# Optimization experiments

Measured on AMD Instinct MI355X. Metric: run time of the kernel, lower is better.

Reference implementation:

```python
import jax, jax.numpy as jnp
import numpy as np

# Dimensions (see shape_source)
B, D, Q, M = 2, 1024, 1024, 1024
K = Q + M                      # klen = mlen + qlen
N_HEAD, D_HEAD = 16, 64        # n_head * d_head == d_model
D_INNER = 4096
LOCAL_SIZE = 1000              # Attention: self.local_size or 1000
EPS = 1e-5                     # F.layer_norm default eps


def setup_inputs() -> dict:
    key = jax.random.key(0)
    ks = jax.random.split(key, 12)
    z = jax.random.normal(ks[0], (B, D, Q), jnp.float32)
    z_hist = jax.random.normal(ks[1], (B, D, M), jnp.float32)
    u = jax.random.normal(ks[2], (B, 3 * N_HEAD * D_HEAD, K), jnp.float32) * 0.1
    # sinusoidal relative position embedding (PositionalEmbedding), positions K-1..0
    inv_freq = 1.0 / (10000.0 ** (jnp.arange(0, D, 2, dtype=jnp.float32) / D))
    pos_seq = jnp.arange(K - 1, -1, -1, dtype=jnp.float32)
    sinusoid = inv_freq[:, None] * pos_seq[None, :]  # (D/2, K)
    pos_emb = jnp.concatenate([jnp.sin(sinusoid), jnp.cos(sinusoid)], axis=0)[None]  # (1, D, K)
    s = 0.02
    W_qkv = jax.random.normal(ks[3], (3 * N_HEAD * D_HEAD, D), jnp.float32) * s
    W_r = jax.random.normal(ks[4], (N_HEAD * D_HEAD, D), jnp.float32) * s
    r_w_bias = jax.random.uniform(ks[5], (N_HEAD, D_HEAD), jnp.float32, -0.05, 0.05)
    r_r_bias = jax.random.uniform(ks[6], (N_HEAD, D_HEAD), jnp.float32, -0.05, 0.05)
    W_o = jax.random.normal(ks[7], (D, N_HEAD * D_HEAD), jnp.float32) * s
    b_o = jnp.zeros((D,), jnp.float32)
    W_ff1 = jax.random.normal(ks[8], (D_INNER, D), jnp.float32) * s
    b_ff1 = jnp.zeros((D_INNER,), jnp.float32)
    W_ff2 = jax.random.normal(ks[9], (D, D_INNER), jnp.float32) * s
    b_ff2 = jnp.zeros((D,), jnp.float32)
    return dict(z=z, z_hist=z_hist, u=u, pos_emb=pos_emb, W_qkv=W_qkv, W_r=W_r,
                r_w_bias=r_w_bias, r_r_bias=r_r_bias, W_o=W_o, b_o=b_o,
                W_ff1=W_ff1, b_ff1=b_ff1, W_ff2=W_ff2, b_ff2=b_ff2)


def _ln(x, axis):
    # F.layer_norm without affine params
    mu = jnp.mean(x, axis=axis, keepdims=True)
    var = jnp.var(x, axis=axis, keepdims=True)
    return (x - mu) / jnp.sqrt(var + EPS)


def _rel_shift(x):
    # Transformer-XL relative shift: pad left on key dim, reinterpret, drop row.
    b, n, q, k = x.shape
    x = jnp.pad(x, ((0, 0), (0, 0), (0, 0), (1, 0)))
    x = x.reshape(b, n, k + 1, q)
    return x[:, :, 1:, :].reshape(b, n, q, k)


def reference(z, z_hist, u, pos_emb, W_qkv, W_r, r_w_bias, r_r_bias, W_o, b_o,
              W_ff1, b_ff1, W_ff2, b_ff2):
    scale = 1.0 / (D_HEAD ** 0.5)
    # ---- Attention (post-LN, Conv1d kernel=1 == pointwise matmul) ----
    cat = jnp.concatenate([z_hist, z], axis=2)                 # (B, D, K)
    w_heads = jnp.einsum('od,bdk->bok', W_qkv, cat) + u        # (B, 3*n*dh, K)
    q_h, k_h, v_h = jnp.split(w_heads, 3, axis=1)
    q_h = q_h[:, :, -Q:].reshape(B, N_HEAD, D_HEAD, Q)
    k_h = k_h.reshape(B, N_HEAD, D_HEAD, K)
    v_h = v_h.reshape(B, N_HEAD, D_HEAD, K)
    r_k = jnp.einsum('od,dk->ok', W_r, pos_emb[0]).reshape(N_HEAD, D_HEAD, K)
    AC = jnp.einsum('bndi,bndj->bnij', q_h + r_w_bias[:, :, None], k_h)
    BD = _rel_shift(jnp.einsum('bndi,ndj->bnij', q_h + r_r_bias[:, :, None], r_k))
    score = (AC + BD) * scale                                  # (B, n, Q, K)
    causal = jnp.triu(jnp.ones((Q, K), bool), k=1 + M)         # future tokens
    local = jnp.tril(jnp.ones((Q, K), bool), k=M - LOCAL_SIZE)  # beyond local window
    mask = causal | local
    score = jnp.where(mask[None, None], -jnp.inf, score)
    prob = jax.nn.softmax(score, axis=-1)
    attn_vec = jnp.einsum('bnij,bndj->bndi', prob, v_h).reshape(B, N_HEAD * D_HEAD, Q)
    attn_out = jnp.einsum('od,bdq->boq', W_o, attn_vec) + b_o[None, :, None]
    out = _ln(attn_out + z, axis=1)                            # LN over d_model (dim=1)
    # ---- FFN (operates token-major) ----
    h = out.transpose(0, 2, 1)                                 # (B, Q, D)
    ff = jnp.maximum(h @ W_ff1.T + b_ff1, 0.0) @ W_ff2.T + b_ff2
    y = _ln(ff + h, axis=-1)
    return y.transpose(0, 2, 1)                                # (B, D, Q)
```

## Files before the change

kernel.cpp:

```cpp
#include <hip/hip_runtime.h>

#define D_MODEL 1024
#define QLEN 1024

typedef __bf16 bf16x8 __attribute__((ext_vector_type(8)));
typedef __bf16 bf16x4 __attribute__((ext_vector_type(4)));
typedef float f32x4 __attribute__((ext_vector_type(4)));

__device__ __forceinline__ void gload16(const void* g, void* l) {
    __builtin_amdgcn_global_load_lds(
        (const __attribute__((address_space(1))) void*)g,
        (__attribute__((address_space(3))) void*)l, 16, 0, 0);
}

__device__ __forceinline__ void gemm_core8(
    __bf16* __restrict__ smA, __bf16* __restrict__ smB,
    const __bf16* __restrict__ A, const __bf16* __restrict__ Bt,
    float* __restrict__ C, __bf16* __restrict__ Cb,
    const float* __restrict__ U, const float* __restrict__ Ut,
    const float* __restrict__ bias,
    int K, int lda, int ldb, int ldC, int ldU, int relu, int m0, int n0)
{
    const int t = threadIdx.x;
    const int lane = t & 63, w = t >> 6;
    const int l15 = lane & 15, lg = lane >> 4;
    const int wm = w >> 2, wn = w & 3;
    const int srow = lane >> 3, cpr = lane & 7;
    const int NK = K >> 6;
    const int SZ = 128 * 64;

    #define STAGE(buf, kt)                                                                   \
    {                                                                                        \
        int k0s = (kt) * 64;                                                                 \
        _Pragma("unroll")                                                                    \
        for (int i = 0; i < 2; ++i) {                                                        \
            int r = w * 16 + i * 8 + srow;                                                   \
            int c = cpr ^ (r & 7);                                                           \
            gload16(&A[(long long)(m0 + r) * lda + k0s + c * 8],                             \
                    &smA[(buf) * SZ + (w * 16 + i * 8) * 64]);                               \
            gload16(&Bt[(long long)(n0 + r) * ldb + k0s + c * 8],                            \
                    &smB[(buf) * SZ + (w * 16 + i * 8) * 64]);                               \
        }                                                                                    \
    }

    f32x4 acc[4][2] = {};
    STAGE(0, 0);

    for (int kt = 0; kt < NK; ++kt) {
        const int cb = kt & 1;
        if (kt + 1 < NK) {
            STAGE(cb ^ 1, kt + 1);
            asm volatile("s_waitcnt vmcnt(4)" ::: "memory");
        } else {
            asm volatile("s_waitcnt vmcnt(0)" ::: "memory");
        }
        __builtin_amdgcn_sched_barrier(0);
        __builtin_amdgcn_s_barrier();

        #pragma unroll
        for (int kk = 0; kk < 2; ++kk) {
            bf16x8 bfr[2];
            #pragma unroll
            for (int nt = 0; nt < 2; ++nt) {
                int nr = wn * 32 + nt * 16 + l15;
                bfr[nt] = *(const bf16x8*)&smB[cb * SZ + nr * 64 + (((kk * 4 + lg) ^ (nr & 7)) * 8)];
            }
            #pragma unroll
            for (int mt = 0; mt < 4; ++mt) {
                int mr = wm * 64 + mt * 16 + l15;
                bf16x8 afr = *(const bf16x8*)&smA[cb * SZ + mr * 64 + (((kk * 4 + lg) ^ (mr & 7)) * 8)];
                #pragma unroll
                for (int nt = 0; nt < 2; ++nt)
                    acc[mt][nt] = __builtin_amdgcn_mfma_f32_16x16x32_bf16(afr, bfr[nt], acc[mt][nt], 0, 0, 0);
            }
        }
        asm volatile("s_waitcnt lgkmcnt(0)" ::: "memory");
        __builtin_amdgcn_sched_barrier(0);
        __builtin_amdgcn_s_barrier();
    }
    #undef STAGE

    if (Ut) {
        float* uf = (float*)smA;
        #pragma unroll
        for (int hh = 0; hh < 2; ++hh) {
            __syncthreads();
            int r = t >> 3, c0 = (t & 7) * 16;
            const float* src = &Ut[(long long)(n0 + hh * 64 + r) * ldU + m0 + c0];
            #pragma unroll
            for (int k = 0; k < 4; ++k)
                *(float4*)&uf[r * 132 + c0 + k * 4] = *(const float4*)&src[k * 4];
            __syncthreads();
            if ((wn >> 1) == hh) {
                #pragma unroll
                for (int nt = 0; nt < 2; ++nt) {
                    int rr = wn * 32 + nt * 16 + l15 - hh * 64;
                    #pragma unroll
                    for (int mt = 0; mt < 4; ++mt) {
                        #pragma unroll
                        for (int rg = 0; rg < 4; ++rg) {
                            int m = wm * 64 + mt * 16 + lg * 4 + rg;
                            acc[mt][nt][rg] += uf[rr * 132 + m];
                        }
                    }
                }
            }
        }
    }

    #pragma unroll
    for (int mt = 0; mt < 4; ++mt) {
        #pragma unroll
        for (int nt = 0; nt < 2; ++nt) {
            #pragma unroll
            for (int rg = 0; rg < 4; ++rg) {
                int m = m0 + wm * 64 + mt * 16 + lg * 4 + rg;
                int n = n0 + wn * 32 + nt * 16 + l15;
                float v = acc[mt][nt][rg];
                if (U)    v += U[(long long)m * ldU + n];
                if (bias) v += bias[n];
                if (relu) v = fmaxf(v, 0.0f);
                if (Cb) Cb[(long long)m * ldC + n] = (__bf16)v;
                else    C [(long long)m * ldC + n] = v;
            }
        }
    }
}

template<int KSPLIT>
__global__ __launch_bounds__(512) void gemm_bf16_k(
    const __bf16* __restrict__ A, const __bf16* __restrict__ Bt,
    float* __restrict__ C0, float* __restrict__ C1,
    __bf16* __restrict__ Cb,
    const float* __restrict__ U, const float* __restrict__ bias,
    int K, int lda, int ldb, int ldC, int ldU, int relu)
{
    __shared__ __bf16 SM[32768];
    int yb = blockIdx.y;
    int half = 0;
    if (KSPLIT > 1) { half = yb & (KSPLIT - 1); yb /= KSPLIT; }
    const int Keff = K / KSPLIT;
    A  += (long long)half * Keff;
    Bt += (long long)half * Keff;
    float* C = half ? C1 : C0;
    if (half) { bias = nullptr; U = nullptr; }
    gemm_core8(SM, SM + 16384, A, Bt, C, Cb, U, nullptr, bias,
               Keff, lda, ldb, ldC, ldU, relu, yb * 128, blockIdx.x * 128);
}

__global__ __launch_bounds__(512) void gemm_fused3(
    const __bf16* __restrict__ cat_t, const __bf16* __restrict__ Wqkvb,
    __bf16* __restrict__ qkT, const float* __restrict__ u,
    __bf16* __restrict__ wh_v,
    const __bf16* __restrict__ pos_t, const __bf16* __restrict__ Wrb,
    __bf16* __restrict__ rkT)
{
    __shared__ __bf16 SM[32768];
    int bid = blockIdx.x;
    if (bid < 512) {
        int zz = bid >> 8, rem = bid & 255, y = rem >> 4, x = rem & 15;
        gemm_core8(SM, SM + 16384,
                   cat_t + (long long)zz * 2097152, Wqkvb,
                   nullptr, qkT + (long long)zz * 4194304,
                   nullptr, u + (long long)zz * 6291456, nullptr,
                   1024, 1024, 1024, 2048, 2048, 0, y * 128, x * 128);
    } else if (bid < 768) {
        int l = bid - 512, zz = l >> 7, rem = l & 127, y = rem >> 4, x = rem & 15;
        gemm_core8(SM, SM + 16384,
                   Wqkvb + 2048 * 1024, cat_t + (long long)zz * 2097152,
                   nullptr, wh_v + (long long)zz * 2097152,
                   u + 4194304 + (long long)zz * 6291456, nullptr, nullptr,
                   1024, 1024, 1024, 2048, 2048, 0, y * 128, x * 128);
    } else {
        int l = bid - 768, y = l >> 3, x = l & 7;
        gemm_core8(SM, SM + 16384,
                   pos_t + 960 * 1024, Wrb,
                   nullptr, rkT, nullptr, nullptr, nullptr,
                   1024, 1024, 1024, 1024, 0, 0, y * 128, x * 128);
    }
}

__global__ __launch_bounds__(256) void prep_all(
    const float* __restrict__ Wqkv, __bf16* __restrict__ Wqkvb,
    const float* __restrict__ Wr,   __bf16* __restrict__ Wrb,
    const float* __restrict__ Wo,   __bf16* __restrict__ Wob,
    const float* __restrict__ Wff1, __bf16* __restrict__ Wff1b,
    const float* __restrict__ Wff2, __bf16* __restrict__ Wff2b,
    const float* __restrict__ zh, const float* __restrict__ z, __bf16* __restrict__ cat_t,
    const float* __restrict__ pos, __bf16* __restrict__ pos_t)
{
    __shared__ float ts[32][33];
    int bid = blockIdx.x;
    const int t = threadIdx.x;
    if (bid < 13312) {
        long long i = ((long long)bid * 256 + t) * 4;
        const float* s; __bf16* dd;
        if (i < 3145728)                    { s = Wqkv + i; dd = Wqkvb + i; }
        else if ((i -= 3145728) < 1048576)  { s = Wr + i;   dd = Wrb + i; }
        else if ((i -= 1048576) < 1048576)  { s = Wo + i;   dd = Wob + i; }
        else if ((i -= 1048576) < 4194304)  { s = Wff1 + i; dd = Wff1b + i; }
        else { i -= 4194304;                  s = Wff2 + i; dd = Wff2b + i; }
        float4 v = *(const float4*)s;
        bf16x4 o = { (__bf16)v.x, (__bf16)v.y, (__bf16)v.z, (__bf16)v.w };
        *(bf16x4*)dd = o;
        return;
    }
    bid -= 13312;
    const float* S; __bf16* D; int R, Cc, bx, by;
    if (bid < 2048) {
        int zz = bid >> 10, r2 = bid & 1023;
        S = zh + (long long)zz * 1048576; D = cat_t + (long long)zz * 2097152;
        R = 1024; Cc = 1024; bx = r2 & 31; by = r2 >> 5;
    } else if (bid < 4096) {
        int l = bid - 2048; int zz = l >> 10, r2 = l & 1023;
        S = z + (long long)zz * 1048576; D = cat_t + 1048576 + (long long)zz * 2097152;
        R = 1024; Cc = 1024; bx = r2 & 31; by = r2 >> 5;
    } else if (bid < 6144) {
        int l = bid - 4096;
        S = pos; D = pos_t; R = 1024; Cc = 2048; bx = l & 63; by = l >> 6;
    } else {
        int l = bid - 6144;
        int i = (l * 256 + t) * 4;
        bf16x4 zv = { (__bf16)0.f, (__bf16)0.f, (__bf16)0.f, (__bf16)0.f };
        *(bf16x4*)&pos_t[2048 * 1024 + i] = zv;
        return;
    }
    int r0 = by * 32, c0 = bx * 32;
    int tr = t >> 5, tc = t & 31;
    #pragma unroll
    for (int p = 0; p < 4; ++p)
        ts[tr + p * 8][tc] = S[(long long)(r0 + tr + p * 8) * Cc + c0 + tc];
    __syncthreads();
    #pragma unroll
    for (int p = 0; p < 4; ++p)
        D[(long long)(c0 + tr + p * 8) * R + r0 + tc] = (__bf16)ts[tc][tr + p * 8];
}

__global__ __launch_bounds__(512) void attn_mfma(
    const __bf16* __restrict__ QKT, const __bf16* __restrict__ WHV,
    const __bf16* __restrict__ RKT,
    const float* __restrict__ rwb, const float* __restrict__ rrb,
    __bf16* __restrict__ AVt)
{
    __shared__ __bf16 SM[51712];
    __bf16* KT0 = SM;
    __bf16* KT1 = SM + 4096;
    __bf16* VS0 = SM + 8192;
    __bf16* VS1 = SM + 12288;
    __bf16* RT  = SM + 16384;
    __bf16* PS  = SM + 32768;
    __bf16* BT  = SM + 40960;

    const int d = blockIdx.x;
    const int xcd = d & 7, idx = d >> 3;
    const int qt = idx & 7;
    const int gq = xcd + 8 * (idx >> 3);
    const int b = gq >> 4, n = gq & 15;
    const int i0 = qt * 128;

    const int t = threadIdx.x;
    const int lane = t & 63, w = t >> 6;
    const int l15 = lane & 15, lg = lane >> 4;
    const int g = w >> 2, wg = w & 3;
    const int fco = n * 64;

    const __bf16* qkb = QKT + (long long)b * (2048 * 2048);
    const __bf16* vb  = WHV + (long long)b * (1024 * 2048) + (long long)fco * 2048;
    __bf16* BTw = BT + w * 1344;

    #pragma unroll
    for (int pp = 0; pp < 2; ++pp) {
        int cid = pp * 512 + t;
        int q = cid >> 3, s = cid & 7, c = s ^ (q & 7);
        bf16x8 qv = *(const bf16x8*)&qkb[(long long)(1024 + i0 + q) * 2048 + fco + c * 8];
        bf16x8 ow, orr;
        #pragma unroll
        for (int e = 0; e < 8; ++e) {
            float qf = (float)qv[e];
            ow[e]  = (__bf16)(qf + rwb[fco + c * 8 + e]);
            orr[e] = (__bf16)(qf + rrb[fco + c * 8 + e]);
        }
        *(bf16x8*)&PS[q * 64 + s * 8] = ow;
        *(bf16x8*)&RT[q * 64 + s * 8] = orr;
    }
    __syncthreads();

    #define LDF(buf, row, ch) (*(const bf16x8*)&(buf)[(row) * 64 + ((((ch) ^ ((row) & 7))) * 8)])

    const int mrow = w * 16 + l15;
    bf16x8 qw0 = LDF(PS, mrow, lg), qw1 = LDF(PS, mrow, lg + 4);
    bf16x8 qr0 = LDF(RT, mrow, lg), qr1 = LDF(RT, mrow, lg + 4);
    asm volatile("s_waitcnt lgkmcnt(0)" ::: "memory");
    __builtin_amdgcn_sched_barrier(0);
    __builtin_amdgcn_s_barrier();

    {
        int r = t >> 3, s = t & 7, c = s ^ (r & 7);
        gload16(&qkb[(long long)(i0 + r) * 2048 + 1024 + fco + c * 8], &KT0[(w * 8) * 64]);
        gload16(&vb[(long long)r * 2048 + i0 + c * 8], &VS0[(w * 8) * 64]);
        #pragma unroll
        for (int pp = 0; pp < 3; ++pp) {
            int cid = pp * 512 + t;
            int rr = cid >> 3, ss = cid & 7, cc = ss ^ (rr & 7);
            gload16(&RKT[(long long)rr * 1024 + fco + cc * 8], &RT[(pp * 64 + w * 8) * 64]);
        }
    }
    asm volatile("s_waitcnt vmcnt(0)" ::: "memory");
    __builtin_amdgcn_sched_barrier(0);
    __builtin_amdgcn_s_barrier();

    const bf16x8 ones = { (__bf16)1.f, (__bf16)1.f, (__bf16)1.f, (__bf16)1.f,
                          (__bf16)1.f, (__bf16)1.f, (__bf16)1.f, (__bf16)1.f };

    f32x4 O0 = {}, O1 = {}, O2 = {}, O3 = {};
    float rm[4] = {-1e30f, -1e30f, -1e30f, -1e30f};
    float rl[4] = {0.f, 0.f, 0.f, 0.f};
    int cur = 0;

    for (int kt = 0; kt <= 17; ++kt) {
        __bf16* KTc = cur ? KT1 : KT0;
        __bf16* VSc = cur ? VS1 : VS0;
        __bf16* KTn = cur ? KT0 : KT1;
        __bf16* VSn = cur ? VS0 : VS1;
        const int ktr = kt - g;

        if (kt < 17) {
            int j0n = i0 + (kt + 1) * 64;
            int r = t >> 3, s = t & 7, c = s ^ (r & 7);
            gload16(&qkb[(long long)(j0n + r) * 2048 + 1024 + fco + c * 8], &KTn[(w * 8) * 64]);
            gload16(&vb[(long long)r * 2048 + j0n + c * 8], &VSn[(w * 8) * 64]);
        }
        if (kt < 16) {
            int rb = kt * 64 + 128;
            int lb = ((kt + 2) & 3) * 64;
            int r = t >> 3, s = t & 7, c = s ^ (r & 7);
            gload16(&RKT[(long long)(rb + r) * 1024 + fco + c * 8], &RT[(lb + w * 8) * 64]);
        }
        __builtin_amdgcn_sched_barrier(0);

        __builtin_amdgcn_s_setprio(1);
        #pragma unroll
        for (int k5 = 0; k5 < 5; ++k5) {
            int pr = (3 - wg + k5) * 16 + l15;
            int lr = ((ktr * 64) + pr) & 255;
            const __bf16* rrow = &RT[lr * 64];
            f32x4 cc = {};
            cc = __builtin_amdgcn_mfma_f32_16x16x32_bf16(qr0, *(const bf16x8*)&rrow[((lg ^ (pr & 7)) * 8)], cc, 0, 0, 0);
            cc = __builtin_amdgcn_mfma_f32_16x16x32_bf16(qr1, *(const bf16x8*)&rrow[(((lg + 4) ^ (pr & 7)) * 8)], cc, 0, 0, 0);
            #pragma unroll
            for (int rg = 0; rg < 4; ++rg)
                BTw[(lg * 4 + rg) * 84 + k5 * 16 + l15] = (__bf16)cc[rg];
        }
        __builtin_amdgcn_s_setprio(0);

        f32x4 cc4[4];
        __builtin_amdgcn_s_setprio(1);
        #pragma unroll
        for (int nt = 0; nt < 4; ++nt) {
            int jr = nt * 16 + l15;
            f32x4 cc = {};
            cc = __builtin_amdgcn_mfma_f32_16x16x32_bf16(qw0, LDF(KTc, jr, lg), cc, 0, 0, 0);
            cc = __builtin_amdgcn_mfma_f32_16x16x32_bf16(qw1, LDF(KTc, jr, lg + 4), cc, 0, 0, 0);
            cc4[nt] = cc;
        }
        __builtin_amdgcn_s_setprio(0);

        const bool bnd = (ktr <= 1) | (ktr >= 16);
        float sv[4][4];
        if (!bnd) {
            #pragma unroll
            for (int nt = 0; nt < 4; ++nt) {
                int jr = nt * 16 + l15;
                #pragma unroll
                for (int rg = 0; rg < 4; ++rg) {
                    int r4 = lg * 4 + rg;
                    sv[nt][rg] = (cc4[nt][rg] + (float)BTw[r4 * 84 + jr - r4 + 15]) * 0.125f;
                }
            }
        } else {
            #pragma unroll
            for (int nt = 0; nt < 4; ++nt) {
                int jr = nt * 16 + l15;
                #pragma unroll
                for (int rg = 0; rg < 4; ++rg) {
                    int r4 = lg * 4 + rg;
                    int dji = jr - (wg * 16 + r4);
                    float s = (cc4[nt][rg] + (float)BTw[r4 * 84 + jr - r4 + 15]) * 0.125f;
                    bool valid = (ktr == 0) ? (dji >= 25)
                               : (ktr == 1) ? (dji >= -39)
                               : (ktr == 16) ? (dji <= 0) : false;
                    sv[nt][rg] = valid ? s : -1e30f;
                }
            }
        }

        float lmax[4];
        bool need = false;
        #pragma unroll
        for (int rg = 0; rg < 4; ++rg) {
            lmax[rg] = fmaxf(fmaxf(sv[0][rg], sv[1][rg]), fmaxf(sv[2][rg], sv[3][rg]));
            need = need || (lmax[rg] > rm[rg] + 8.0f);
        }
        if (__any(need)) {
            #pragma unroll
            for (int rg = 0; rg < 4; ++rg) {
                float m = lmax[rg];
                m = fmaxf(m, __shfl_xor(m, 1, 16));
                m = fmaxf(m, __shfl_xor(m, 2, 16));
                m = fmaxf(m, __shfl_xor(m, 4, 16));
                m = fmaxf(m, __shfl_xor(m, 8, 16));
                float nm = fmaxf(rm[rg], m);
                float fac = __expf(rm[rg] - nm);
                rm[rg] = nm;
                rl[rg] *= fac;
                O0[rg] *= fac; O1[rg] *= fac; O2[rg] *= fac; O3[rg] *= fac;
            }
        }

        if (!bnd) {
            #pragma unroll
            for (int nt = 0; nt < 4; ++nt) {
                int jc = nt * 16 + l15;
                #pragma unroll
                for (int rg = 0; rg < 4; ++rg) {
                    float p = __expf(sv[nt][rg] - rm[rg]);
                    int row = w * 16 + lg * 4 + rg;
                    PS[row * 64 + (((jc >> 3) ^ (row & 7)) * 8) + (jc & 7)] = (__bf16)p;
                }
            }
        } else {
            #pragma unroll
            for (int nt = 0; nt < 4; ++nt) {
                int jc = nt * 16 + l15;
                #pragma unroll
                for (int rg = 0; rg < 4; ++rg) {
                    float p = (sv[nt][rg] > -1e29f) ? __expf(sv[nt][rg] - rm[rg]) : 0.0f;
                    int row = w * 16 + lg * 4 + rg;
                    PS[row * 64 + (((jc >> 3) ^ (row & 7)) * 8) + (jc & 7)] = (__bf16)p;
                }
            }
        }

        bf16x8 pa0 = LDF(PS, mrow, lg), pa1 = LDF(PS, mrow, lg + 4);
        f32x4 Os = {};
        __builtin_amdgcn_s_setprio(1);
        Os = __builtin_amdgcn_mfma_f32_16x16x32_bf16(pa0, ones, Os, 0, 0, 0);
        Os = __builtin_amdgcn_mfma_f32_16x16x32_bf16(pa1, ones, Os, 0, 0, 0);
        O0 = __builtin_amdgcn_mfma_f32_16x16x32_bf16(pa0, LDF(VSc,  0 + l15, lg),     O0, 0, 0, 0);
        O0 = __builtin_amdgcn_mfma_f32_16x16x32_bf16(pa1, LDF(VSc,  0 + l15, lg + 4), O0, 0, 0, 0);
        O1 = __builtin_amdgcn_mfma_f32_16x16x32_bf16(pa0, LDF(VSc, 16 + l15, lg),     O1, 0, 0, 0);
        O1 = __builtin_amdgcn_mfma_f32_16x16x32_bf16(pa1, LDF(VSc, 16 + l15, lg + 4), O1, 0, 0, 0);
        O2 = __builtin_amdgcn_mfma_f32_16x16x32_bf16(pa0, LDF(VSc, 32 + l15, lg),     O2, 0, 0, 0);
        O2 = __builtin_amdgcn_mfma_f32_16x16x32_bf16(pa1, LDF(VSc, 32 + l15, lg + 4), O2, 0, 0, 0);
        O3 = __builtin_amdgcn_mfma_f32_16x16x32_bf16(pa0, LDF(VSc, 48 + l15, lg),     O3, 0, 0, 0);
        O3 = __builtin_amdgcn_mfma_f32_16x16x32_bf16(pa1, LDF(VSc, 48 + l15, lg + 4), O3, 0, 0, 0);
        __builtin_amdgcn_s_setprio(0);
        #pragma unroll
        for (int rg = 0; rg < 4; ++rg) rl[rg] += Os[rg];

        asm volatile("s_waitcnt vmcnt(0)" ::: "memory");
        __builtin_amdgcn_sched_barrier(0);
        __builtin_amdgcn_s_barrier();
        cur ^= 1;
    }

    #pragma unroll
    for (int rg = 0; rg < 4; ++rg) {
        float inv = 1.0f / rl[rg];
        int q = i0 + w * 16 + lg * 4 + rg;
        long long base = ((long long)b * 1024 + q) * 1024 + fco;
        AVt[base +  0 + l15] = (__bf16)(O0[rg] * inv);
        AVt[base + 16 + l15] = (__bf16)(O1[rg] * inv);
        AVt[base + 32 + l15] = (__bf16)(O2[rg] * inv);
        AVt[base + 48 + l15] = (__bf16)(O3[rg] * inv);
    }
    #undef LDF
}

__global__ __launch_bounds__(256) void ln1_kernel(
    const float* __restrict__ A0, const float* __restrict__ A1,
    const float* __restrict__ bo, const __bf16* __restrict__ CatT,
    __bf16* __restrict__ Hb)
{
    int i = blockIdx.x, b = blockIdx.y, t = threadIdx.x;
    __shared__ float xs[D_MODEL];
    __shared__ float red[256];
    __shared__ float smu, srstd;
    long long tb = ((long long)b * 1024 + i) * 1024;
    long long zb = ((long long)b * 2048 + 1024 + i) * 1024;

    float lsum = 0.0f;
    for (int dd = t; dd < D_MODEL; dd += 256) {
        float v = A0[tb + dd] + A1[tb + dd] + bo[dd] + (float)CatT[zb + dd];
        xs[dd] = v;
        lsum += v;
    }
    red[t] = lsum; __syncthreads();
    for (int s2 = 128; s2 > 0; s2 >>= 1) { if (t < s2) red[t] += red[t + s2]; __syncthreads(); }
    if (t == 0) smu = red[0] * (1.0f / D_MODEL);
    __syncthreads();
    float mu = smu;

    float lq = 0.0f;
    for (int dd = t; dd < D_MODEL; dd += 256) { float c = xs[dd] - mu; lq += c * c; }
    red[t] = lq; __syncthreads();
    for (int s2 = 128; s2 > 0; s2 >>= 1) { if (t < s2) red[t] += red[t + s2]; __syncthreads(); }
    if (t == 0) srstd = rsqrtf(red[0] * (1.0f / D_MODEL) + 1e-5f);
    __syncthreads();
    float rstd = srstd;

    for (int dd = t; dd < D_MODEL; dd += 256)
        Hb[tb + dd] = (__bf16)((xs[dd] - mu) * rstd);
}

__global__ __launch_bounds__(256) void ln2_stats(
    const float* __restrict__ F0, const float* __restrict__ F1,
    const __bf16* __restrict__ Hb, float2* __restrict__ st)
{
    int i = blockIdx.x, b = blockIdx.y, t = threadIdx.x;
    __shared__ float rs[256], rq[256];
    long long tb = ((long long)b * 1024 + i) * 1024;

    float s = 0.f, q = 0.f;
    for (int dd = t; dd < D_MODEL; dd += 256) {
        float v = F0[tb + dd] + F1[tb + dd] + (float)Hb[tb + dd];
        s += v; q += v * v;
    }
    rs[t] = s; rq[t] = q; __syncthreads();
    for (int s2 = 128; s2 > 0; s2 >>= 1) {
        if (t < s2) { rs[t] += rs[t + s2]; rq[t] += rq[t + s2]; }
        __syncthreads();
    }
    if (t == 0) {
        float mu = rs[0] * (1.0f / D_MODEL);
        float var = rq[0] * (1.0f / D_MODEL) - mu * mu;
        st[(long long)b * 1024 + i] = make_float2(mu, rsqrtf(var + 1e-5f));
    }
}

__global__ __launch_bounds__(256) void ln2_write(
    const float* __restrict__ F0, const float* __restrict__ F1,
    const __bf16* __restrict__ Hb, const float2* __restrict__ st,
    float* __restrict__ OUT)
{
    __shared__ float ts[32][33];
    int f0 = blockIdx.x * 32, i0 = blockIdx.y * 32, b = blockIdx.z;
    int tr = threadIdx.x >> 5, tc = threadIdx.x & 31;
    #pragma unroll
    for (int p = 0; p < 4; ++p) {
        int tok = i0 + tr + p * 8;
        long long tb = ((long long)b * 1024 + tok) * 1024;
        float2 s = st[(long long)b * 1024 + tok];
        float v = F0[tb + f0 + tc] + F1[tb + f0 + tc] + (float)Hb[tb + f0 + tc];
        ts[tr + p * 8][tc] = (v - s.x) * s.y;
    }
    __syncthreads();
    #pragma unroll
    for (int p = 0; p < 4; ++p)
        OUT[((long long)b * 1024 + f0 + tr + p * 8) * 1024 + i0 + tc] = ts[tc][tr + p * 8];
}

extern "C" void kernel_launch(void* const* d_in, const int* in_sizes, int n_in,
                              void* d_out, int out_size, void* d_ws, size_t ws_size,
                              hipStream_t stream) {
    const float* z    = (const float*)d_in[0];
    const float* zh   = (const float*)d_in[1];
    const float* u    = (const float*)d_in[2];
    const float* pos  = (const float*)d_in[3];
    const float* Wqkv = (const float*)d_in[4];
    const float* Wr   = (const float*)d_in[5];
    const float* rwb  = (const float*)d_in[6];
    const float* rrb  = (const float*)d_in[7];
    const float* Wo   = (const float*)d_in[8];
    const float* bo   = (const float*)d_in[9];
    const float* Wff1 = (const float*)d_in[10];
    const float* bff1 = (const float*)d_in[11];
    const float* Wff2 = (const float*)d_in[12];
    const float* bff2 = (const float*)d_in[13];
    float* out = (float*)d_out;
    float* ws  = (float*)d_ws;

    __bf16* cat_t = (__bf16*)ws;
    __bf16* pos_t = (__bf16*)(ws + 2097152);
    __bf16* Wqkvb = (__bf16*)(ws + 3178496);
    __bf16* Wrb   = (__bf16*)(ws + 4751360);
    __bf16* Wob   = (__bf16*)(ws + 5275648);
    __bf16* Wff1b = (__bf16*)(ws + 5799936);
    __bf16* Wff2b = (__bf16*)(ws + 7897088);
    __bf16* qkT   = (__bf16*)(ws + 14188544);
    __bf16* wh_v  = (__bf16*)(ws + 18382848);
    __bf16* rkT   = (__bf16*)(ws + 20480000);
    __bf16* av_t  = (__bf16*)(ws + 21069824);
    float*  ao0   = ws + 22118400;
    float*  ao1   = ws + 24215552;
    __bf16* h_bf  = (__bf16*)(ws + 26312704);
    float2* st2   = (float2*)(ws + 27361280);
    __bf16* f1b   = (__bf16*)(ws + 14188544);
    float*  f20   = ws + 9994240;
    float*  f21   = ws + 12091392;

    prep_all<<<19520, 256, 0, stream>>>(
        Wqkv, Wqkvb, Wr, Wrb, Wo, Wob, Wff1, Wff1b, Wff2, Wff2b,
        zh, z, cat_t, pos, pos_t);

    gemm_fused3<<<840, 512, 0, stream>>>(
        cat_t, Wqkvb, qkT, u, wh_v, pos_t, Wrb, rkT);

    attn_mfma<<<256, 512, 0, stream>>>(qkT, wh_v, rkT, rwb, rrb, av_t);

    gemm_bf16_k<2><<<dim3(8, 32, 1), 512, 0, stream>>>(
        av_t, Wob, ao0, ao1, nullptr, nullptr, nullptr,
        1024, 1024, 1024, 1024, 0, 0);
    ln1_kernel<<<dim3(1024, 2), 256, 0, stream>>>(ao0, ao1, bo, cat_t, h_bf);
    gemm_bf16_k<1><<<dim3(32, 16, 1), 512, 0, stream>>>(
        h_bf, Wff1b, nullptr, nullptr, f1b, nullptr, bff1,
        1024, 1024, 1024, 4096, 0, 1);
    gemm_bf16_k<2><<<dim3(8, 32, 1), 512, 0, stream>>>(
        f1b, Wff2b, f20, f21, nullptr, nullptr, bff2,
        4096, 4096, 4096, 1024, 0, 0);
    ln2_stats<<<dim3(1024, 2), 256, 0, stream>>>(f20, f21, h_bf, st2);
    ln2_write<<<dim3(32, 32, 2), 256, 0, stream>>>(f20, f21, h_bf, st2, out);
}
```

Measured before the change: 204.1 us.

## Use 4-stage K=32 pipelined GEMM core with single barrier in fused QKV kernel

Adds a new GEMM core variant for the fused QKV/position projection kernel. It uses K-tiles of 32 instead of 64 and a four-buffer ring with three tiles prefetched ahead, a new XOR swizzle for the 32-wide rows, and one barrier per iteration instead of two. It also raises wave priority around the MFMA block. The aim is to hide global-to-LDS latency and cut barrier stalls, at the cost of more loop iterations and smaller MFMA batches per barrier. The original core stays in use for the other GEMM kernels.

```diff
diff --git a/kernel.cpp b/kernel.cpp
--- a/kernel.cpp
+++ b/kernel.cpp
@@ -13,7 +13,7 @@
         (__attribute__((address_space(3))) void*)l, 16, 0, 0);
 }
 
-__device__ __forceinline__ void gemm_core8(
+__device__ __forceinline__ void gemm_core8p3(
     __bf16* __restrict__ smA, __bf16* __restrict__ smB,
     const __bf16* __restrict__ A, const __bf16* __restrict__ Bt,
     float* __restrict__ C, __bf16* __restrict__ Cb,
@@ -25,60 +25,50 @@
     const int lane = t & 63, w = t >> 6;
     const int l15 = lane & 15, lg = lane >> 4;
     const int wm = w >> 2, wn = w & 3;
-    const int srow = lane >> 3, cpr = lane & 7;
-    const int NK = K >> 6;
-    const int SZ = 128 * 64;
-
-    #define STAGE(buf, kt)                                                                   \
-    {                                                                                        \
-        int k0s = (kt) * 64;                                                                 \
-        _Pragma("unroll")                                                                    \
-        for (int i = 0; i < 2; ++i) {                                                        \
-            int r = w * 16 + i * 8 + srow;                                                   \
-            int c = cpr ^ (r & 7);                                                           \
-            gload16(&A[(long long)(m0 + r) * lda + k0s + c * 8],                             \
-                    &smA[(buf) * SZ + (w * 16 + i * 8) * 64]);                               \
-            gload16(&Bt[(long long)(n0 + r) * ldb + k0s + c * 8],                            \
-                    &smB[(buf) * SZ + (w * 16 + i * 8) * 64]);                               \
-        }                                                                                    \
+    const int NK = K >> 5;
+    const int ABUF = 4096;
+
+    const int srow = w * 16 + (lane >> 2);
+    const int scol = (lane & 3) ^ ((srow >> 1) & 3);
+
+    #define STAGE3(buf, kt)                                                     \
+    {                                                                           \
+        int k0s = (kt) * 32;                                                    \
+        gload16(&A[(long long)(m0 + srow) * lda + k0s + scol * 8],              \
+                &smA[(buf) * ABUF + (w * 16) * 32]);                            \
+        gload16(&Bt[(long long)(n0 + srow) * ldb + k0s + scol * 8],             \
+                &smB[(buf) * ABUF + (w * 16) * 32]);                            \
     }
 
     f32x4 acc[4][2] = {};
-    STAGE(0, 0);
+    STAGE3(0, 0); STAGE3(1, 1); STAGE3(2, 2);
 
     for (int kt = 0; kt < NK; ++kt) {
-        const int cb = kt & 1;
-        if (kt + 1 < NK) {
-            STAGE(cb ^ 1, kt + 1);
-            asm volatile("s_waitcnt vmcnt(4)" ::: "memory");
-        } else {
-            asm volatile("s_waitcnt vmcnt(0)" ::: "memory");
-        }
+        const int cb = kt & 3;
+        if (kt + 2 < NK)      asm volatile("s_waitcnt vmcnt(4) lgkmcnt(0)" ::: "memory");
+        else if (kt + 1 < NK) asm volatile("s_waitcnt vmcnt(2) lgkmcnt(0)" ::: "memory");
+        else                  asm volatile("s_waitcnt vmcnt(0) lgkmcnt(0)" ::: "memory");
         __builtin_amdgcn_sched_barrier(0);
         __builtin_amdgcn_s_barrier();
-
-        #pragma unroll
-        for (int kk = 0; kk < 2; ++kk) {
-            bf16x8 bfr[2];
-            #pragma unroll
-            for (int nt = 0; nt < 2; ++nt) {
-                int nr = wn * 32 + nt * 16 + l15;
-                bfr[nt] = *(const bf16x8*)&smB[cb * SZ + nr * 64 + (((kk * 4 + lg) ^ (nr & 7)) * 8)];
-            }
-            #pragma unroll
-            for (int mt = 0; mt < 4; ++mt) {
-                int mr = wm * 64 + mt * 16 + l15;
-                bf16x8 afr = *(const bf16x8*)&smA[cb * SZ + mr * 64 + (((kk * 4 + lg) ^ (mr & 7)) * 8)];
-                #pragma unroll
-                for (int nt = 0; nt < 2; ++nt)
-                    acc[mt][nt] = __builtin_amdgcn_mfma_f32_16x16x32_bf16(afr, bfr[nt], acc[mt][nt], 0, 0, 0);
-            }
-        }
-        asm volatile("s_waitcnt lgkmcnt(0)" ::: "memory");
-        __builtin_amdgcn_sched_barrier(0);
-        __builtin_amdgcn_s_barrier();
-    }
-    #undef STAGE
+        if (kt + 3 < NK) STAGE3((kt + 3) & 3, kt + 3);
+
+        bf16x8 bfr[2];
+        #pragma unroll
+        for (int nt = 0; nt < 2; ++nt) {
+            int nr = wn * 32 + nt * 16 + l15;
+            bfr[nt] = *(const bf16x8*)&smB[cb * ABUF + nr * 32 + ((lg ^ ((nr >> 1) & 3)) * 8)];
+        }
+        __builtin_amdgcn_s_setprio(1);
+        #pragma unroll
+        for (int mt = 0; mt < 4; ++mt) {
+            int mr = wm * 64 + mt * 16 + l15;
+            bf16x8 afr = *(const bf16x8*)&smA[cb * ABUF + mr * 32 + ((lg ^ ((mr >> 1) & 3)) * 8)];
+            acc[mt][0] = __builtin_amdgcn_mfma_f32_16x16x32_bf16(afr, bfr[0], acc[mt][0], 0, 0, 0);
+            acc[mt][1] = __builtin_amdgcn_mfma_f32_16x16x32_bf16(afr, bfr[1], acc[mt][1], 0, 0, 0);
+        }
+        __builtin_amdgcn_s_setprio(0);
+    }
+    #undef STAGE3
 
     if (Ut) {
         float* uf = (float*)smA;
@@ -127,6 +117,92 @@
     }
 }
 
+__device__ __forceinline__ void gemm_core8(
+    __bf16* __restrict__ smA, __bf16* __restrict__ smB,
+    const __bf16* __restrict__ A, const __bf16* __restrict__ Bt,
+    float* __restrict__ C, __bf16* __restrict__ Cb,
+    const float* __restrict__ U, const float* __restrict__ Ut,
+    const float* __restrict__ bias,
+    int K, int lda, int ldb, int ldC, int ldU, int relu, int m0, int n0)
+{
+    const int t = threadIdx.x;
+    const int lane = t & 63, w = t >> 6;
+    const int l15 = lane & 15, lg = lane >> 4;
+    const int wm = w >> 2, wn = w & 3;
+    const int srow = lane >> 3, cpr = lane & 7;
+    const int NK = K >> 6;
+    const int SZ = 128 * 64;
+
+    #define STAGE(buf, kt)                                                                   \
+    {                                                                                        \
+        int k0s = (kt) * 64;                                                                 \
+        _Pragma("unroll")                                                                    \
+        for (int i = 0; i < 2; ++i) {                                                        \
+            int r = w * 16 + i * 8 + srow;                                                   \
+            int c = cpr ^ (r & 7);                                                           \
+            gload16(&A[(long long)(m0 + r) * lda + k0s + c * 8],                             \
+                    &smA[(buf) * SZ + (w * 16 + i * 8) * 64]);                               \
+            gload16(&Bt[(long long)(n0 + r) * ldb + k0s + c * 8],                            \
+                    &smB[(buf) * SZ + (w * 16 + i * 8) * 64]);                               \
+        }                                                                                    \
+    }
+
+    f32x4 acc[4][2] = {};
+    STAGE(0, 0);
+
+    for (int kt = 0; kt < NK; ++kt) {
+        const int cb = kt & 1;
+        if (kt + 1 < NK) {
+            STAGE(cb ^ 1, kt + 1);
+            asm volatile("s_waitcnt vmcnt(4)" ::: "memory");
+        } else {
+            asm volatile("s_waitcnt vmcnt(0)" ::: "memory");
+        }
+        __builtin_amdgcn_sched_barrier(0);
+        __builtin_amdgcn_s_barrier();
+
+        #pragma unroll
+        for (int kk = 0; kk < 2; ++kk) {
+            bf16x8 bfr[2];
+            #pragma unroll
+            for (int nt = 0; nt < 2; ++nt) {
+                int nr = wn * 32 + nt * 16 + l15;
+                bfr[nt] = *(const bf16x8*)&smB[cb * SZ + nr * 64 + (((kk * 4 + lg) ^ (nr & 7)) * 8)];
+            }
+            #pragma unroll
+            for (int mt = 0; mt < 4; ++mt) {
+                int mr = wm * 64 + mt * 16 + l15;
+                bf16x8 afr = *(const bf16x8*)&smA[cb * SZ + mr * 64 + (((kk * 4 + lg) ^ (mr & 7)) * 8)];
+                #pragma unroll
+                for (int nt = 0; nt < 2; ++nt)
+                    acc[mt][nt] = __builtin_amdgcn_mfma_f32_16x16x32_bf16(afr, bfr[nt], acc[mt][nt], 0, 0, 0);
+            }
+        }
+        asm volatile("s_waitcnt lgkmcnt(0)" ::: "memory");
+        __builtin_amdgcn_sched_barrier(0);
+        __builtin_amdgcn_s_barrier();
+    }
+    #undef STAGE
+
+    #pragma unroll
+    for (int mt = 0; mt < 4; ++mt) {
+        #pragma unroll
+        for (int nt = 0; nt < 2; ++nt) {
+            #pragma unroll
+            for (int rg = 0; rg < 4; ++rg) {
+                int m = m0 + wm * 64 + mt * 16 + lg * 4 + rg;
+                int n = n0 + wn * 32 + nt * 16 + l15;
+                float v = acc[mt][nt][rg];
+                if (U)    v += U[(long long)m * ldU + n];
+                if (bias) v += bias[n];
+                if (relu) v = fmaxf(v, 0.0f);
+                if (Cb) Cb[(long long)m * ldC + n] = (__bf16)v;
+                else    C [(long long)m * ldC + n] = v;
+            }
+        }
+    }
+}
+
 template<int KSPLIT>
 __global__ __launch_bounds__(512) void gemm_bf16_k(
     const __bf16* __restrict__ A, const __bf16* __restrict__ Bt,
@@ -159,24 +235,24 @@
     int bid = blockIdx.x;
     if (bid < 512) {
         int zz = bid >> 8, rem = bid & 255, y = rem >> 4, x = rem & 15;
-        gemm_core8(SM, SM + 16384,
-                   cat_t + (long long)zz * 2097152, Wqkvb,
-                   nullptr, qkT + (long long)zz * 4194304,
-                   nullptr, u + (long long)zz * 6291456, nullptr,
-                   1024, 1024, 1024, 2048, 2048, 0, y * 128, x * 128);
+        gemm_core8p3(SM, SM + 16384,
+                     cat_t + (long long)zz * 2097152, Wqkvb,
+                     nullptr, qkT + (long long)zz * 4194304,
+                     nullptr, u + (long long)zz * 6291456, nullptr,
+                     1024, 1024, 1024, 2048, 2048, 0, y * 128, x * 128);
     } else if (bid < 768) {
         int l = bid - 512, zz = l >> 7, rem = l & 127, y = rem >> 4, x = rem & 15;
-        gemm_core8(SM, SM + 16384,
-                   Wqkvb + 2048 * 1024, cat_t + (long long)zz * 2097152,
-                   nullptr, wh_v + (long long)zz * 2097152,
-                   u + 4194304 + (long long)zz * 6291456, nullptr, nullptr,
-                   1024, 1024, 1024, 2048, 2048, 0, y * 128, x * 128);
+        gemm_core8p3(SM, SM + 16384,
+                     Wqkvb + 2048 * 1024, cat_t + (long long)zz * 2097152,
+                     nullptr, wh_v + (long long)zz * 2097152,
+                     u + 4194304 + (long long)zz * 6291456, nullptr, nullptr,
+                     1024, 1024, 1024, 2048, 2048, 0, y * 128, x * 128);
     } else {
         int l = bid - 768, y = l >> 3, x = l & 7;
-        gemm_core8(SM, SM + 16384,
-                   pos_t + 960 * 1024, Wrb,
-                   nullptr, rkT, nullptr, nullptr, nullptr,
-                   1024, 1024, 1024, 1024, 0, 0, y * 128, x * 128);
+        gemm_core8p3(SM, SM + 16384,
+                     pos_t + 960 * 1024, Wrb,
+                     nullptr, rkT, nullptr, nullptr, nullptr,
+                     1024, 1024, 1024, 1024, 0, 0, y * 128, x * 128);
     }
 }
 
```

New measurement: 208.1 us. Within noise of the previous version (+2.0%).
